# Kernel optimization log

Hardware: AMD Instinct MI355X
Metric: run time of the kernel (lower is better)

The kernel has to match this reference:

```python
import jax, jax.numpy as jnp
import numpy as np

THRESH = 0.5
BETA = 0.25


def setup_inputs() -> dict:
    key = jax.random.key(0)
    # [T, B, C, H, W] time-major spiking CNN activations
    x = jax.random.normal(key, (8, 32, 128, 32, 32), dtype=jnp.float32)
    return {"x": x}


def reference(x) -> jnp.ndarray:
    """Leaky integrate-and-fire scan over the leading time axis.

    mem[t] = beta * mem[t-1] + x[t]
    s[t]   = heaviside(mem[t] - thresh)
    mem[t] <- mem[t] * (1 - s[t])   # hard reset after spike
    Returns spikes with the same shape as x.
    """

    def step(mem, xt):
        mem = mem * BETA + xt
        spk = (mem >= THRESH).astype(xt.dtype)
        mem = mem * (1.0 - spk)  # hard reset
        return mem, spk

    mem0 = jnp.zeros_like(x[0])
    _, spikes = jax.lax.scan(step, mem0, x)
    return spikes
```

## Files before the change

kernel.cpp:

```cpp
#include <hip/hip_runtime.h>


#define LIF_THRESH 0.5f
#define LIF_BETA   0.25f
#define LIF_T      8
#define BLOCK      256
#define JITER      8

typedef float v4f __attribute__((ext_vector_type(4)));

__global__ __launch_bounds__(BLOCK) void lif_kernel(const v4f* __restrict__ x,
                                                    v4f* __restrict__ out,
                                                    int n4) {
    const int base = blockIdx.x * (BLOCK * JITER) + threadIdx.x;

    v4f cur[LIF_T], nxt[LIF_T];

#pragma unroll
    for (int t = 0; t < LIF_T; ++t)
        cur[t] = __builtin_nontemporal_load(&x[(size_t)t * n4 + base]);

#pragma unroll
    for (int j = 0; j < JITER; ++j) {
        const int c = base + j * BLOCK;

        if (j + 1 < JITER) {
            const int cn = c + BLOCK;
#pragma unroll
            for (int t = 0; t < LIF_T; ++t)
                nxt[t] = __builtin_nontemporal_load(&x[(size_t)t * n4 + cn]);
        }

        float m0 = 0.f, m1 = 0.f, m2 = 0.f, m3 = 0.f;
#pragma unroll
        for (int t = 0; t < LIF_T; ++t) {
            v4f xt = cur[t];
            m0 = m0 * LIF_BETA + xt.x;
            m1 = m1 * LIF_BETA + xt.y;
            m2 = m2 * LIF_BETA + xt.z;
            m3 = m3 * LIF_BETA + xt.w;

            v4f s;
            s.x = (m0 >= LIF_THRESH) ? 1.f : 0.f;
            s.y = (m1 >= LIF_THRESH) ? 1.f : 0.f;
            s.z = (m2 >= LIF_THRESH) ? 1.f : 0.f;
            s.w = (m3 >= LIF_THRESH) ? 1.f : 0.f;

            m0 = (m0 >= LIF_THRESH) ? 0.f : m0;
            m1 = (m1 >= LIF_THRESH) ? 0.f : m1;
            m2 = (m2 >= LIF_THRESH) ? 0.f : m2;
            m3 = (m3 >= LIF_THRESH) ? 0.f : m3;

            __builtin_nontemporal_store(s, &out[(size_t)t * n4 + c]);
        }

        if (j + 1 < JITER) {
#pragma unroll
            for (int t = 0; t < LIF_T; ++t) cur[t] = nxt[t];
        }
    }
}

extern "C" void kernel_launch(void* const* d_in, const int* in_sizes, int n_in,
                              void* d_out, int out_size, void* d_ws, size_t ws_size,
                              hipStream_t stream) {
    const v4f* x = (const v4f*)d_in[0];
    v4f* out = (v4f*)d_out;

    long long total = in_sizes[0];
    int n = (int)(total / LIF_T);
    int n4 = n / 4;

    dim3 block(BLOCK);
    dim3 grid(n4 / (BLOCK * JITER));
    lif_kernel<<<grid, block, 0, stream>>>(x, out, n4);
}
```

Before: 224.6 us.

## Stage input through LDS with async global_load_lds double buffering

Loads each time-step row with direct global-to-LDS async loads into a double-buffered shared tile, one wave per time step. Each thread then runs the LIF scan over two columns from LDS and writes spikes back in place, and each wave streams its row of results out. The aim is to keep more loads in flight with fewer registers and better-overlapped prefetch. In exchange it adds barriers, LDS traffic and hand-written vmcnt waits that must match the exact issue counts.

Result: no change. 224.8 us (+0.1%).

```diff
diff --git a/kernel.cpp b/kernel.cpp
--- a/kernel.cpp
+++ b/kernel.cpp
@@ -4,61 +4,89 @@
 #define LIF_THRESH 0.5f
 #define LIF_BETA   0.25f
 #define LIF_T      8
-#define BLOCK      256
-#define JITER      8
+#define BLOCK      512
+#define TILE_W     256
+#define TILES      8
 
 typedef float v4f __attribute__((ext_vector_type(4)));
+typedef float v2f __attribute__((ext_vector_type(2)));
+
+template <int N>
+__device__ __forceinline__ void wait_vmcnt() {
+    asm volatile("s_waitcnt vmcnt(%0)" ::"n"(N) : "memory");
+}
+__device__ __forceinline__ void wait_lgkmcnt0() {
+    asm volatile("s_waitcnt lgkmcnt(0)" ::: "memory");
+}
+__device__ __forceinline__ void barrier_fenced() {
+    asm volatile("s_barrier" ::: "memory");
+}
 
 __global__ __launch_bounds__(BLOCK) void lif_kernel(const v4f* __restrict__ x,
                                                     v4f* __restrict__ out,
                                                     int n4) {
-    const int base = blockIdx.x * (BLOCK * JITER) + threadIdx.x;
+    __shared__ v4f xs[2][LIF_T][TILE_W];
 
-    v4f cur[LIF_T], nxt[LIF_T];
+    const int wave = threadIdx.x >> 6;
+    const int lane = threadIdx.x & 63;
+    const size_t col0  = (size_t)blockIdx.x * (TILE_W * TILES);
+    const size_t gbase = (size_t)wave * (size_t)n4 + col0;
+
+#define STAGE(tile, buf)                                                       \
+    {                                                                          \
+        _Pragma("unroll")                                                      \
+        for (int i = 0; i < TILE_W / 64; ++i) {                                \
+            __builtin_amdgcn_global_load_lds(                                  \
+                (const __attribute__((address_space(1))) void*)                \
+                    (&x[gbase + (size_t)(tile)*TILE_W + i * 64 + lane]),       \
+                (__attribute__((address_space(3))) void*)                      \
+                    (&xs[buf][wave][i * 64]),                                  \
+                16, 0, 2 );           \
+        }                                                                      \
+    }
+
+    STAGE(0, 0);
 
 #pragma unroll
-    for (int t = 0; t < LIF_T; ++t)
-        cur[t] = __builtin_nontemporal_load(&x[(size_t)t * n4 + base]);
+    for (int k = 0; k < TILES; ++k) {
+        const int buf = k & 1;
+
+        if (k + 1 < TILES) STAGE(k + 1, buf ^ 1);
+
+        if (k == 0)             wait_vmcnt<4>();
+        else if (k + 1 < TILES) wait_vmcnt<8>();
+        else                    wait_vmcnt<4>();
+        barrier_fenced();
+
+        {
+            const int ci = threadIdx.x;
+            float m0 = 0.f, m1 = 0.f;
+#pragma unroll
+            for (int t = 0; t < LIF_T; ++t) {
+                v2f xv = ((const v2f*)xs[buf][t])[ci];
+                m0 = m0 * LIF_BETA + xv.x;
+                m1 = m1 * LIF_BETA + xv.y;
+                v2f s;
+                s.x = (m0 >= LIF_THRESH) ? 1.f : 0.f;
+                s.y = (m1 >= LIF_THRESH) ? 1.f : 0.f;
+                m0 = (m0 >= LIF_THRESH) ? 0.f : m0;
+                m1 = (m1 >= LIF_THRESH) ? 0.f : m1;
+                ((v2f*)xs[buf][t])[ci] = s;
+            }
+        }
+
+        wait_lgkmcnt0();
+        __builtin_amdgcn_sched_barrier(0);
+        barrier_fenced();
 
 #pragma unroll
-    for (int j = 0; j < JITER; ++j) {
-        const int c = base + j * BLOCK;
-
-        if (j + 1 < JITER) {
-            const int cn = c + BLOCK;
-#pragma unroll
-            for (int t = 0; t < LIF_T; ++t)
-                nxt[t] = __builtin_nontemporal_load(&x[(size_t)t * n4 + cn]);
-        }
-
-        float m0 = 0.f, m1 = 0.f, m2 = 0.f, m3 = 0.f;
-#pragma unroll
-        for (int t = 0; t < LIF_T; ++t) {
-            v4f xt = cur[t];
-            m0 = m0 * LIF_BETA + xt.x;
-            m1 = m1 * LIF_BETA + xt.y;
-            m2 = m2 * LIF_BETA + xt.z;
-            m3 = m3 * LIF_BETA + xt.w;
-
-            v4f s;
-            s.x = (m0 >= LIF_THRESH) ? 1.f : 0.f;
-            s.y = (m1 >= LIF_THRESH) ? 1.f : 0.f;
-            s.z = (m2 >= LIF_THRESH) ? 1.f : 0.f;
-            s.w = (m3 >= LIF_THRESH) ? 1.f : 0.f;
-
-            m0 = (m0 >= LIF_THRESH) ? 0.f : m0;
-            m1 = (m1 >= LIF_THRESH) ? 0.f : m1;
-            m2 = (m2 >= LIF_THRESH) ? 0.f : m2;
-            m3 = (m3 >= LIF_THRESH) ? 0.f : m3;
-
-            __builtin_nontemporal_store(s, &out[(size_t)t * n4 + c]);
-        }
-
-        if (j + 1 < JITER) {
-#pragma unroll
-            for (int t = 0; t < LIF_T; ++t) cur[t] = nxt[t];
+        for (int i = 0; i < TILE_W / 64; ++i) {
+            v4f s = xs[buf][wave][i * 64 + lane];
+            __builtin_nontemporal_store(
+                s, &out[gbase + (size_t)k * TILE_W + i * 64 + lane]);
         }
     }
+#undef STAGE
 }
 
 extern "C" void kernel_launch(void* const* d_in, const int* in_sizes, int n_in,
@@ -72,6 +100,6 @@
     int n4 = n / 4;
 
     dim3 block(BLOCK);
-    dim3 grid(n4 / (BLOCK * JITER));
+    dim3 grid(n4 / (TILE_W * TILES));
     lif_kernel<<<grid, block, 0, stream>>>(x, out, n4);
 }
```
